# Kernel tuning notes

Measured on AMD Instinct MI355X. Metric: run time of the kernel, lower is better.

The kernel has to match this reference:

```python
import jax, jax.numpy as jnp
import numpy as np

EPS = 1e-5

def _ln(x):
    # F.layer_norm over last dim, no affine params
    m = jnp.mean(x, axis=-1, keepdims=True)
    v = jnp.mean((x - m) ** 2, axis=-1, keepdims=True)
    return (x - m) * jax.lax.rsqrt(v + EPS)

def _jagged_to_padded(vals, offsets, B, n):
    # vals: [T, F] -> [B, n, F], zero padded
    T = vals.shape[0]
    lengths = offsets[1:] - offsets[:-1]            # [B]
    pos = jnp.arange(n)
    idx = offsets[:-1, None] + pos[None, :]         # [B, n]
    valid = pos[None, :] < lengths[:, None]         # [B, n]
    gathered = vals[jnp.clip(idx, 0, T - 1)]        # [B, n, F]
    return jnp.where(valid[..., None], gathered, 0.0)

def _dense_to_jagged(padded, offsets, T):
    # padded: [B, n, F] -> [T, F]
    t = jnp.arange(T)
    b = jnp.clip(jnp.searchsorted(offsets, t, side='right') - 1, 0, offsets.shape[0] - 2)
    pos = t - offsets[b]
    return padded[b, pos]

def setup_inputs() -> dict:
    key = jax.random.key(0)
    D, H, d = 1024, 8, 128
    B, n = 4, 2048
    T = B * n  # all sequences full length
    ks = jax.random.split(key, 4)
    x = jax.random.normal(ks[0], (T, D), dtype=jnp.float32)
    attnmask = jnp.tril(jnp.ones((n, n), dtype=jnp.float32))
    x_offsets = jnp.arange(B + 1, dtype=jnp.int32) * n
    proj_w = jax.random.normal(ks[1], (D, H * d * 4), dtype=jnp.float32) * 0.02
    out_w = jax.random.normal(ks[2], (H * d, D), dtype=jnp.float32) * 0.02
    out_b = jnp.zeros((D,), dtype=jnp.float32)
    return {"x": x, "attnmask": attnmask, "proj_w": proj_w, "out_w": out_w,
            "out_b": out_b, "x_offsets": x_offsets, "B": B, "n": n}

def reference(x, attnmask, proj_w, out_w, out_b, x_offsets, B, n):
    T, D = x.shape
    H, d4 = 8, proj_w.shape[1] // 8
    d = d4 // 4
    x = _ln(x)
    h = jax.nn.silu(x @ proj_w).reshape(T, H, 4 * d)   # silu BEFORE split (HSTU)
    u, v, q, k = jnp.split(h, 4, axis=-1)              # each [T, H, d]
    pq = _jagged_to_padded(q.reshape(T, H * d), x_offsets, B, n).reshape(B, n, H, d)
    pk = _jagged_to_padded(k.reshape(T, H * d), x_offsets, B, n).reshape(B, n, H, d)
    pv = _jagged_to_padded(v.reshape(T, H * d), x_offsets, B, n).reshape(B, n, H, d)
    scores = jnp.einsum('bnhd,bmhd->bhnm', pq, pk)
    scores = jax.nn.silu(scores) / n * attnmask[None, None]
    attnout = jnp.einsum('bhnm,bmhd->bnhd', scores, pv).reshape(B, n, H * d)
    attnout = _dense_to_jagged(attnout, x_offsets, T)  # [T, H*d]
    attnout = _ln(attnout) * u.reshape(T, H * d)       # fused norm + gate
    return attnout @ out_w + out_b                      # out_proj (dropout inactive: eval)
```

## Files before the change

kernel.cpp:

```cpp
#include <hip/hip_runtime.h>

typedef short  s16x8 __attribute__((ext_vector_type(8)));
typedef float  f32x4 __attribute__((ext_vector_type(4)));
typedef unsigned short u16;
typedef unsigned int   u32;

#define T_TOK 8192
#define D_IN  1024
#define D4    4096
#define NH    8
#define DH    128
#define NSEQ  2048

__device__ __forceinline__ float u16f(u16 s){
  union { unsigned int u; float f; } c; c.u = ((unsigned int)s) << 16; return c.f;
}
__device__ __forceinline__ u16 f2u16(float f){
  union { float f; unsigned int u; } c; c.f = f;
  unsigned int r = (c.u + 0x7fffu + ((c.u >> 16) & 1u)) >> 16;
  return (u16)r;
}
__device__ __forceinline__ unsigned int cvt2_bf16(float a, float b){
  unsigned int r;
  asm("v_cvt_pk_bf16_f32 %0, %1, %2" : "=v"(r) : "v"(a), "v"(b));
  return r;
}
__device__ __forceinline__ float fast_silu(float v){
  return v * __builtin_amdgcn_rcpf(1.0f + __expf(-v));
}
__device__ __forceinline__ void gload_lds16(const u16* g, u16* lds){
  __builtin_amdgcn_global_load_lds(
      (const __attribute__((address_space(1))) u32*)g,
      (__attribute__((address_space(3))) u32*)lds, 16, 0, 0);
}

__device__ __forceinline__ void block_reduce2(float& a, float& b){
  __shared__ float red[8];
  #pragma unroll
  for (int off = 32; off > 0; off >>= 1){
    a += __shfl_down(a, off, 64);
    b += __shfl_down(b, off, 64);
  }
  int w = threadIdx.x >> 6;
  if ((threadIdx.x & 63) == 0){ red[w*2] = a; red[w*2+1] = b; }
  __syncthreads();
  a = red[0] + red[2] + red[4] + red[6];
  b = red[1] + red[3] + red[5] + red[7];
  __syncthreads();
}

__global__ void ln_x_kernel(const float* __restrict__ x, u16* __restrict__ xn){
  int t = blockIdx.x;
  const float* row = x + (size_t)t * D_IN;
  int base = threadIdx.x * 4;
  float4 v = *(const float4*)(row + base);
  float s = v.x + v.y + v.z + v.w;
  float q = v.x*v.x + v.y*v.y + v.z*v.z + v.w*v.w;
  block_reduce2(s, q);
  float mean = s * (1.0f / D_IN);
  float var  = q * (1.0f / D_IN) - mean * mean;
  float rstd = rsqrtf(var + 1e-5f);
  ushort4 o;
  o.x = f2u16((v.x - mean) * rstd); o.y = f2u16((v.y - mean) * rstd);
  o.z = f2u16((v.z - mean) * rstd); o.w = f2u16((v.w - mean) * rstd);
  *(ushort4*)(xn + (size_t)t * D_IN + base) = o;
}

__global__ void transpose_kernel(const float* __restrict__ in, u16* __restrict__ out,
                                 int R, int C){
  __shared__ u16 tile[32][33];
  int c0 = blockIdx.x * 32, r0 = blockIdx.y * 32;
  for (int i = threadIdx.y; i < 32; i += 8)
    tile[i][threadIdx.x] = f2u16(in[(size_t)(r0 + i) * C + c0 + threadIdx.x]);
  __syncthreads();
  for (int i = threadIdx.y; i < 32; i += 8)
    out[(size_t)(c0 + i) * R + r0 + threadIdx.x] = tile[threadIdx.x][i];
}

__global__ void vt_kernel(const u16* __restrict__ h, u16* __restrict__ vt){
  __shared__ u16 tile[32][33];
  int bh = blockIdx.z; int b = bh >> 3, hh = bh & 7;
  int p0 = blockIdx.x * 32, d0 = blockIdx.y * 32;
  const u16* src = h + (size_t)(b * NSEQ) * D4 + hh * 512 + 128;
  for (int i = threadIdx.y; i < 32; i += 8)
    tile[i][threadIdx.x] = src[(size_t)(p0 + i) * D4 + d0 + threadIdx.x];
  __syncthreads();
  u16* dst = vt + (size_t)bh * DH * NSEQ;
  for (int i = threadIdx.y; i < 32; i += 8)
    dst[(size_t)(d0 + i) * NSEQ + p0 + threadIdx.x] = tile[threadIdx.x][i];
}

template<int EPI>
__global__ __launch_bounds__(256, 2) void gemm_bt_kernel(
    const u16* __restrict__ A, const u16* __restrict__ Bt,
    const float* __restrict__ bias, u16* __restrict__ Cb, float* __restrict__ Cf,
    int M, int N, int K)
{
  __shared__ __align__(16) u16 As[128 * 64];
  __shared__ __align__(16) u16 Bs[128 * 64];
  int bn = blockIdx.x, bm = blockIdx.y;
  int tid = threadIdx.x;
  int lane = tid & 63, wave = tid >> 6;
  int lr = lane & 15, quad = lane >> 4;
  int wm = (wave >> 1) * 64, wn = (wave & 1) * 64;
  f32x4 acc[4][4] = {};

  int srow = lane >> 3;
  int scol = ((lane & 7) ^ srow) * 8;
  const u16* Ab = A  + (size_t)(bm * 128) * K;
  const u16* Bb = Bt + (size_t)(bn * 128) * K;
  int swz = (lr & 7) * 8;

  for (int k0 = 0; k0 < K; k0 += 64){
    #pragma unroll
    for (int it = 0; it < 4; ++it){
      int c = it * 4 + wave;
      gload_lds16(Ab + (size_t)(c * 8 + srow) * K + k0 + scol, As + c * 512);
    }
    #pragma unroll
    for (int it = 0; it < 4; ++it){
      int c = it * 4 + wave;
      gload_lds16(Bb + (size_t)(c * 8 + srow) * K + k0 + scol, Bs + c * 512);
    }
    __syncthreads();
    #pragma unroll
    for (int ks = 0; ks < 2; ++ks){
      s16x8 af[4], bf[4];
      #pragma unroll
      for (int i = 0; i < 4; ++i)
        af[i] = *(const s16x8*)&As[(wm + i*16 + lr) * 64 + (((ks*32 + quad*8)) ^ swz)];
      #pragma unroll
      for (int j = 0; j < 4; ++j)
        bf[j] = *(const s16x8*)&Bs[(wn + j*16 + lr) * 64 + (((ks*32 + quad*8)) ^ swz)];
      #pragma unroll
      for (int i = 0; i < 4; ++i)
        #pragma unroll
        for (int j = 0; j < 4; ++j)
          acc[i][j] = __builtin_amdgcn_mfma_f32_16x16x32_bf16(af[i], bf[j], acc[i][j], 0, 0, 0);
    }
    __syncthreads();
  }
  #pragma unroll
  for (int j = 0; j < 4; ++j){
    int nc = bn * 128 + wn + j * 16 + lr;
    float bv = 0.0f;
    if (EPI == 1) bv = bias[nc];
    #pragma unroll
    for (int i = 0; i < 4; ++i){
      #pragma unroll
      for (int r = 0; r < 4; ++r){
        int mr = bm * 128 + wm + i * 16 + quad * 4 + r;
        float v = acc[i][j][r];
        if (EPI == 0){
          v = fast_silu(v);
          Cb[(size_t)mr * N + nc] = f2u16(v);
        } else {
          Cf[(size_t)mr * N + nc] = v + bv;
        }
      }
    }
  }
}

__global__ __launch_bounds__(512, 4) void attn_kernel(
    const u16* __restrict__ h, const u16* __restrict__ vt, u16* __restrict__ ao)
{
  __shared__ __align__(16) u16 smem[40960];

  int id = blockIdx.x;
  int fl = id & 255;
  int x = fl & 7, y = fl >> 3;
  int bhl = x * 2 + (y & 1);
  int qtr = y >> 1;
  int qt, bh;
  if (id < 256){ bh = bhl;      qt = qtr;      }
  else         { bh = 16 + bhl; qt = 15 - qtr; }
  int b = bh >> 3, hh = bh & 7;
  int tid = threadIdx.x;
  int lane = tid & 63, wave = tid >> 6;
  int lr = lane & 15, quad = lane >> 4;
  int wq = wave * 16;

  const u16* kbase = h  + (size_t)(b * NSEQ) * D4 + hh * 512 + 384;
  const u16* vbase = vt + (size_t)bh * DH * NSEQ;
  u16* Ssl = smem + 32768;

  auto stage = [&](int bufsel, int k0n){
    u16* kd = smem + bufsel * 8192;
    u16* vd = smem + 16384 + bufsel * 8192;
    #pragma unroll
    for (int it = 0; it < 2; ++it){
      int c = it * 8 + wave;
      int row = c * 4 + (lane >> 4);
      int ss = (lane & 15) ^ (row & 15);
      gload_lds16(kbase + (size_t)(k0n + row) * D4 + ss * 8, kd + c * 512);
    }
    #pragma unroll
    for (int it = 0; it < 2; ++it){
      int c = it * 8 + wave;
      int row = c * 8 + (lane >> 3);
      int ss = (lane & 7) ^ (lane >> 3);
      gload_lds16(vbase + (size_t)row * NSEQ + k0n + ss * 8, vd + c * 512);
    }
  };

  const u16* qsrc = h + (size_t)(b * NSEQ + qt * 128) * D4 + hh * 512 + 256;
  s16x8 qf[4];
  #pragma unroll
  for (int ks = 0; ks < 4; ++ks)
    qf[ks] = *(const s16x8*)(qsrc + (size_t)(wq + lr) * D4 + ks*32 + quad*8);

  stage(0, 0);
  __syncthreads();

  f32x4 oacc[8] = {};
  int nkt = 2 * qt + 2;

  for (int kt = 0; kt < nkt; ++kt){
    int cur = kt & 1;
    int k0 = kt * 64;
    if (kt + 1 < nkt) stage(cur ^ 1, k0 + 64);

    const u16* kc = smem + cur * 8192;
    const u16* vc = smem + 16384 + cur * 8192;

    int lk0 = k0 - qt * 128;
    bool active = (lk0 < wq + 16);
    if (active){
      f32x4 sacc[4] = {};
      __builtin_amdgcn_s_setprio(1);
      #pragma unroll
      for (int ks = 0; ks < 4; ++ks){
        s16x8 kf[4];
        #pragma unroll
        for (int jb = 0; jb < 4; ++jb)
          kf[jb] = *(const s16x8*)&kc[(jb*16 + lr) * 128 + (((ks*4 + quad) ^ lr) << 3)];
        #pragma unroll
        for (int jb = 0; jb < 4; ++jb)
          sacc[jb] = __builtin_amdgcn_mfma_f32_16x16x32_bf16(qf[ks], kf[jb], sacc[jb], 0, 0, 0);
      }
      __builtin_amdgcn_s_setprio(0);

      bool needmask = (lk0 + 63 > wq);
      #pragma unroll
      for (int jb = 0; jb < 4; ++jb){
        int qbase = wq + quad*4;
        int slot = jb*2 + (lr >> 3);
        int off  = lr & 7;
        float p[4];
        if (needmask){
          #pragma unroll
          for (int r = 0; r < 4; ++r){
            float v = fast_silu(sacc[jb][r]);
            if (lk0 + jb*16 + lr > qbase + r) v = 0.0f;
            p[r] = v;
          }
        } else {
          #pragma unroll
          for (int r = 0; r < 4; ++r)
            p[r] = fast_silu(sacc[jb][r]);
        }
        unsigned int c01 = cvt2_bf16(p[0], p[1]);
        unsigned int c23 = cvt2_bf16(p[2], p[3]);
        Ssl[(qbase+0)*64 + (((slot ^ ((qbase+0)&7)) << 3) | off)] = (u16)(c01);
        Ssl[(qbase+1)*64 + (((slot ^ ((qbase+1)&7)) << 3) | off)] = (u16)(c01 >> 16);
        Ssl[(qbase+2)*64 + (((slot ^ ((qbase+2)&7)) << 3) | off)] = (u16)(c23);
        Ssl[(qbase+3)*64 + (((slot ^ ((qbase+3)&7)) << 3) | off)] = (u16)(c23 >> 16);
      }

      __builtin_amdgcn_s_setprio(1);
      #pragma unroll
      for (int ks = 0; ks < 2; ++ks){
        s16x8 pf, vf2[8];
        pf = *(const s16x8*)&Ssl[(wq + lr) * 64 + (((ks*4 + quad) ^ (lr & 7)) << 3)];
        #pragma unroll
        for (int j = 0; j < 8; ++j)
          vf2[j] = *(const s16x8*)&vc[(j*16 + lr) * 64 + (((ks*4 + quad) ^ (lr & 7)) << 3)];
        #pragma unroll
        for (int j = 0; j < 8; ++j)
          oacc[j] = __builtin_amdgcn_mfma_f32_16x16x32_bf16(pf, vf2[j], oacc[j], 0, 0, 0);
      }
      __builtin_amdgcn_s_setprio(0);
    }
    __syncthreads();
  }

  u16* aobase = ao + (size_t)(b * NSEQ + qt * 128) * D_IN + hh * DH;
  #pragma unroll
  for (int j = 0; j < 8; ++j){
    float s0 = oacc[j][0] * (1.0f / (float)NSEQ);
    float s1 = oacc[j][1] * (1.0f / (float)NSEQ);
    float s2 = oacc[j][2] * (1.0f / (float)NSEQ);
    float s3 = oacc[j][3] * (1.0f / (float)NSEQ);
    unsigned int c01 = cvt2_bf16(s0, s1);
    unsigned int c23 = cvt2_bf16(s2, s3);
    int rbase = wq + quad*4;
    aobase[(size_t)(rbase+0) * D_IN + j*16 + lr] = (u16)(c01);
    aobase[(size_t)(rbase+1) * D_IN + j*16 + lr] = (u16)(c01 >> 16);
    aobase[(size_t)(rbase+2) * D_IN + j*16 + lr] = (u16)(c23);
    aobase[(size_t)(rbase+3) * D_IN + j*16 + lr] = (u16)(c23 >> 16);
  }
}

__global__ void ln_gate_kernel(const u16* __restrict__ ao, const u16* __restrict__ h,
                               u16* __restrict__ gated){
  int t = blockIdx.x;
  const u16* row = ao + (size_t)t * D_IN;
  int base = threadIdx.x * 4;
  ushort4 raw = *(const ushort4*)(row + base);
  float vx = u16f(raw.x), vy = u16f(raw.y), vz = u16f(raw.z), vw = u16f(raw.w);
  float s = vx + vy + vz + vw;
  float q = vx*vx + vy*vy + vz*vz + vw*vw;
  block_reduce2(s, q);
  float mean = s * (1.0f / D_IN);
  float var  = q * (1.0f / D_IN) - mean * mean;
  float rstd = rsqrtf(var + 1e-5f);
  ushort4 uu = *(const ushort4*)(h + (size_t)t * D4 + (base >> 7) * 512 + (base & 127));
  ushort4 o;
  o.x = f2u16((vx - mean) * rstd * u16f(uu.x));
  o.y = f2u16((vy - mean) * rstd * u16f(uu.y));
  o.z = f2u16((vz - mean) * rstd * u16f(uu.z));
  o.w = f2u16((vw - mean) * rstd * u16f(uu.w));
  *(ushort4*)(gated + (size_t)t * D_IN + base) = o;
}

extern "C" void kernel_launch(void* const* d_in, const int* in_sizes, int n_in,
                              void* d_out, int out_size, void* d_ws, size_t ws_size,
                              hipStream_t stream)
{
  (void)in_sizes; (void)n_in; (void)out_size; (void)ws_size;
  const float* x      = (const float*)d_in[0];
  const float* proj_w = (const float*)d_in[2];
  const float* out_w  = (const float*)d_in[3];
  const float* out_b  = (const float*)d_in[4];
  float* out = (float*)d_out;

  const size_t MB = 1024 * 1024;
  char* ws = (char*)d_ws;
  u16* xn  = (u16*)(ws);
  u16* h   = (u16*)(ws + 16 * MB);
  u16* Wt  = (u16*)(ws + 80 * MB);
  u16* OWt = (u16*)(ws + 88 * MB);
  u16* Vt  = (u16*)(ws + 90 * MB);
  u16* ao    = xn;
  u16* gated = Vt;

  dim3 tb32(32, 8);
  hipLaunchKernelGGL(transpose_kernel, dim3(D4 / 32, D_IN / 32), tb32, 0, stream,
                     proj_w, Wt, D_IN, D4);
  hipLaunchKernelGGL(transpose_kernel, dim3(D_IN / 32, D_IN / 32), tb32, 0, stream,
                     out_w, OWt, D_IN, D_IN);
  hipLaunchKernelGGL(ln_x_kernel, dim3(T_TOK), dim3(256), 0, stream, x, xn);
  hipLaunchKernelGGL(HIP_KERNEL_NAME(gemm_bt_kernel<0>), dim3(D4 / 128, T_TOK / 128),
                     dim3(256), 0, stream, xn, Wt, (const float*)nullptr, h,
                     (float*)nullptr, T_TOK, D4, D_IN);
  hipLaunchKernelGGL(vt_kernel, dim3(NSEQ / 32, DH / 32, 32), tb32, 0, stream, h, Vt);
  hipLaunchKernelGGL(attn_kernel, dim3(512), dim3(512), 0, stream, h, Vt, ao);
  hipLaunchKernelGGL(ln_gate_kernel, dim3(T_TOK), dim3(256), 0, stream, ao, h, gated);
  hipLaunchKernelGGL(HIP_KERNEL_NAME(gemm_bt_kernel<1>), dim3(D_IN / 128, T_TOK / 128),
                     dim3(256), 0, stream, gated, OWt, out_b, (u16*)nullptr,
                     out, T_TOK, D_IN, D_IN);
}
```

Baseline: 309.7 us.

## Fuse V transpose into projection GEMM epilogue and merge weight transposes

The projection GEMM epilogue now writes the V tiles directly in transposed [b,h,d,pos] layout, which removes the separate vt_kernel pass over h. The two weight-transpose launches are merged into one kernel that picks its source by block index. The aim is to cut a 16MB read-plus-write pass and two kernel launches. The trade-off is that transposed stores from the GEMM epilogue are less coalesced and add branching to the epilogue.

```diff
diff --git a/kernel.cpp b/kernel.cpp
--- a/kernel.cpp
+++ b/kernel.cpp
@@ -66,10 +66,14 @@
   *(ushort4*)(xn + (size_t)t * D_IN + base) = o;
 }
 
-__global__ void transpose_kernel(const float* __restrict__ in, u16* __restrict__ out,
-                                 int R, int C){
+__global__ void transpose2_kernel(const float* __restrict__ in0, u16* __restrict__ out0,
+                                  const float* __restrict__ in1, u16* __restrict__ out1){
   __shared__ u16 tile[32][33];
-  int c0 = blockIdx.x * 32, r0 = blockIdx.y * 32;
+  int bx = blockIdx.x;
+  const float* in; u16* out; int R, C, c0;
+  if (bx < 128){ in = in0; out = out0; R = D_IN; C = D4;   c0 = bx * 32; }
+  else         { in = in1; out = out1; R = D_IN; C = D_IN; c0 = (bx - 128) * 32; }
+  int r0 = blockIdx.y * 32;
   for (int i = threadIdx.y; i < 32; i += 8)
     tile[i][threadIdx.x] = f2u16(in[(size_t)(r0 + i) * C + c0 + threadIdx.x]);
   __syncthreads();
@@ -77,24 +81,11 @@
     out[(size_t)(c0 + i) * R + r0 + threadIdx.x] = tile[threadIdx.x][i];
 }
 
-__global__ void vt_kernel(const u16* __restrict__ h, u16* __restrict__ vt){
-  __shared__ u16 tile[32][33];
-  int bh = blockIdx.z; int b = bh >> 3, hh = bh & 7;
-  int p0 = blockIdx.x * 32, d0 = blockIdx.y * 32;
-  const u16* src = h + (size_t)(b * NSEQ) * D4 + hh * 512 + 128;
-  for (int i = threadIdx.y; i < 32; i += 8)
-    tile[i][threadIdx.x] = src[(size_t)(p0 + i) * D4 + d0 + threadIdx.x];
-  __syncthreads();
-  u16* dst = vt + (size_t)bh * DH * NSEQ;
-  for (int i = threadIdx.y; i < 32; i += 8)
-    dst[(size_t)(d0 + i) * NSEQ + p0 + threadIdx.x] = tile[threadIdx.x][i];
-}
-
 template<int EPI>
 __global__ __launch_bounds__(256, 2) void gemm_bt_kernel(
     const u16* __restrict__ A, const u16* __restrict__ Bt,
     const float* __restrict__ bias, u16* __restrict__ Cb, float* __restrict__ Cf,
-    int M, int N, int K)
+    u16* __restrict__ VtOut, int M, int N, int K)
 {
   __shared__ __align__(16) u16 As[128 * 64];
   __shared__ __align__(16) u16 Bs[128 * 64];
@@ -140,22 +131,42 @@
     }
     __syncthreads();
   }
-  #pragma unroll
-  for (int j = 0; j < 4; ++j){
-    int nc = bn * 128 + wn + j * 16 + lr;
-    float bv = 0.0f;
-    if (EPI == 1) bv = bias[nc];
-    #pragma unroll
-    for (int i = 0; i < 4; ++i){
-      #pragma unroll
-      for (int r = 0; r < 4; ++r){
-        int mr = bm * 128 + wm + i * 16 + quad * 4 + r;
-        float v = acc[i][j][r];
-        if (EPI == 0){
-          v = fast_silu(v);
-          Cb[(size_t)mr * N + nc] = f2u16(v);
-        } else {
-          Cf[(size_t)mr * N + nc] = v + bv;
+
+  if (EPI == 0 && (bn & 3) == 1){
+    int hh = bn >> 2, bb = bm >> 4;
+    u16* vtb = VtOut + (size_t)(bb * 8 + hh) * DH * NSEQ;
+    #pragma unroll
+    for (int j = 0; j < 4; ++j){
+      int dd = wn + j * 16 + lr;
+      #pragma unroll
+      for (int i = 0; i < 4; ++i){
+        int pos = (bm & 15) * 128 + wm + i * 16 + quad * 4;
+        ushort4 o;
+        o.x = f2u16(fast_silu(acc[i][j][0]));
+        o.y = f2u16(fast_silu(acc[i][j][1]));
+        o.z = f2u16(fast_silu(acc[i][j][2]));
+        o.w = f2u16(fast_silu(acc[i][j][3]));
+        *(ushort4*)(vtb + (size_t)dd * NSEQ + pos) = o;
+      }
+    }
+  } else {
+    #pragma unroll
+    for (int j = 0; j < 4; ++j){
+      int nc = bn * 128 + wn + j * 16 + lr;
+      float bv = 0.0f;
+      if (EPI == 1) bv = bias[nc];
+      #pragma unroll
+      for (int i = 0; i < 4; ++i){
+        #pragma unroll
+        for (int r = 0; r < 4; ++r){
+          int mr = bm * 128 + wm + i * 16 + quad * 4 + r;
+          float v = acc[i][j][r];
+          if (EPI == 0){
+            v = fast_silu(v);
+            Cb[(size_t)mr * N + nc] = f2u16(v);
+          } else {
+            Cf[(size_t)mr * N + nc] = v + bv;
+          }
         }
       }
     }
@@ -346,18 +357,15 @@
   u16* gated = Vt;
 
   dim3 tb32(32, 8);
-  hipLaunchKernelGGL(transpose_kernel, dim3(D4 / 32, D_IN / 32), tb32, 0, stream,
-                     proj_w, Wt, D_IN, D4);
-  hipLaunchKernelGGL(transpose_kernel, dim3(D_IN / 32, D_IN / 32), tb32, 0, stream,
-                     out_w, OWt, D_IN, D_IN);
+  hipLaunchKernelGGL(transpose2_kernel, dim3(160, 32), tb32, 0, stream,
+                     proj_w, Wt, out_w, OWt);
   hipLaunchKernelGGL(ln_x_kernel, dim3(T_TOK), dim3(256), 0, stream, x, xn);
   hipLaunchKernelGGL(HIP_KERNEL_NAME(gemm_bt_kernel<0>), dim3(D4 / 128, T_TOK / 128),
                      dim3(256), 0, stream, xn, Wt, (const float*)nullptr, h,
-                     (float*)nullptr, T_TOK, D4, D_IN);
-  hipLaunchKernelGGL(vt_kernel, dim3(NSEQ / 32, DH / 32, 32), tb32, 0, stream, h, Vt);
+                     (float*)nullptr, Vt, T_TOK, D4, D_IN);
   hipLaunchKernelGGL(attn_kernel, dim3(512), dim3(512), 0, stream, h, Vt, ao);
   hipLaunchKernelGGL(ln_gate_kernel, dim3(T_TOK), dim3(256), 0, stream, ao, h, gated);
   hipLaunchKernelGGL(HIP_KERNEL_NAME(gemm_bt_kernel<1>), dim3(D_IN / 128, T_TOK / 128),
                      dim3(256), 0, stream, gated, OWt, out_b, (u16*)nullptr,
-                     out, T_TOK, D_IN, D_IN);
-}
+                     out, (u16*)nullptr, T_TOK, D_IN, D_IN);
+}
```

New measurement: 290.0 us. 6.4% less time.
